# Optimization experiments

Hardware: AMD Instinct MI355X
Metric: run time of the kernel (lower is better)

## Reference

```python
import jax, jax.numpy as jnp
import numpy as np

V = 5023      # CoMA mesh vertices
K = 8         # avg neighbors per vertex
E = V * K     # edges
B = 64        # batch
C_IN = 3      # xyz
C_HID = 64    # conv width (layer_info)
M = 9         # kernel_size: number of weight matrices
LATENT = 128


def fsc_conv(x, src, dst, aw, u, c, W, b):
    """Feature-steered graph conv (translation invariant: v = -u).
    x: [B,V,C]; edge e: (i=src[e], j=dst[e]) with adjacency weight aw[e].
    y_i = b + sum_j a_ij * sum_m softmax_m(u_m.(x_i-x_j)+c_m) * (x_j @ W_m)
    """
    Bx, Vx, C = x.shape
    D = W.shape[2]
    xi = x[:, src]                                  # [B,E,C]
    xj = x[:, dst]                                  # [B,E,C]
    logits = jnp.einsum('bec,cm->bem', xi - xj, u) + c   # [B,E,M]
    att = jax.nn.softmax(logits, axis=-1) * aw[None, :, None]
    y = jnp.zeros((Bx, Vx, D), x.dtype)
    for m in range(W.shape[0]):                     # small fixed loop over M
        agg = jnp.zeros((Bx, Vx, C), x.dtype).at[:, src].add(att[:, :, m:m + 1] * xj)
        y = y + agg @ W[m]
    return y + b


def setup_inputs() -> dict:
    key = jax.random.key(0)
    ks = jax.random.split(key, 16)
    x = jax.random.normal(ks[0], (B, V, C_IN), jnp.float32)
    # mesh-like adjacency: each vertex i has K random neighbors, weight 1/K
    src = jnp.repeat(jnp.arange(V, dtype=jnp.int32), K)
    dst = jax.random.randint(ks[1], (E,), 0, V, dtype=jnp.int32)
    aw = jnp.full((E,), 1.0 / K, jnp.float32)
    g = lambda k, shp, fan: jax.random.normal(k, shp, jnp.float32) * np.float32(np.sqrt(2.0 / fan))
    # encoder conv params
    u_e = g(ks[2], (C_IN, M), C_IN + M)
    c_e = jnp.zeros((M,), jnp.float32)
    W_e = g(ks[3], (M, C_IN, C_HID), C_IN + C_HID)
    b_e = jnp.zeros((C_HID,), jnp.float32)
    # encoder latent dense: [V*C_HID, LATENT]
    W_enc = g(ks[4], (V * C_HID, LATENT), V * C_HID)
    b_enc = jnp.zeros((LATENT,), jnp.float32)
    # decoder latent dense: [LATENT, C_HID*V]
    W_dec = g(ks[5], (LATENT, C_HID * V), LATENT)
    b_dec = jnp.zeros((C_HID * V,), jnp.float32)
    # decoder conv params
    u_d = g(ks[6], (C_HID, M), C_HID + M)
    c_d = jnp.zeros((M,), jnp.float32)
    W_d = g(ks[7], (M, C_HID, C_IN), C_HID + C_IN)
    b_d = jnp.zeros((C_IN,), jnp.float32)
    return {'x': x, 'aw': aw, 'u_e': u_e, 'c_e': c_e, 'W_e': W_e, 'b_e': b_e,
            'W_enc': W_enc, 'b_enc': b_enc, 'W_dec': W_dec, 'b_dec': b_dec,
            'u_d': u_d, 'c_d': c_d, 'W_d': W_d, 'b_d': b_d,
            'src': src, 'dst': dst}


def reference(x, aw, u_e, c_e, W_e, b_e, W_enc, b_enc, W_dec, b_dec,
              u_d, c_d, W_d, b_d, src, dst):
    # Encoder: feature-steered conv -> relu -> flatten -> dense to latent
    h = jax.nn.relu(fsc_conv(x, src, dst, aw, u_e, c_e, W_e, b_e))   # [B,V,C_HID]
    z = h.reshape(h.shape[0], -1) @ W_enc + b_enc                    # [B,LATENT]
    # Decoder: dense -> reshape [B,V,C_HID] -> feature-steered conv -> relu
    d = (z @ W_dec + b_dec).reshape(z.shape[0], V, -1)               # [B,V,C_HID]
    out = jax.nn.relu(fsc_conv(d, src, dst, aw, u_d, c_d, W_d, b_d)) # [B,V,3]
    return out
```

## Files before the change

kernel.cpp:

```cpp
#include <hip/hip_runtime.h>

#define VN 5023
#define KN 8
#define BN 64
#define CIN 3
#define CH 64
#define MN 9
#define LAT 128
#define KTOT (VN*CH)
#define NBV (BN*VN)
#define KC 256
#define NCHUNK 1256
#define RED_G 8
#define RED_J 157
#define NXCD 8
#define DEC_TILES 1256
#define DEC_GRID 512

__global__ __launch_bounds__(256, 4) void k_conv1(
    const float* __restrict__ x, const float* __restrict__ aw,
    const int* __restrict__ dst,
    const float* __restrict__ u_e, const float* __restrict__ c_e,
    const float* __restrict__ W_e, const float* __restrict__ b_e,
    float* __restrict__ h)
{
  int t = blockIdx.x*256 + threadIdx.x;
  if (t >= NBV) return;
  int b = t / VN, v = t - b*VN;
  const float* xb = x + (size_t)b*VN*CIN;
  int e0 = v*KN;
  int4 j01 = *(const int4*)(dst + e0);
  int4 j23 = *(const int4*)(dst + e0 + 4);
  int jj[8] = {j01.x,j01.y,j01.z,j01.w, j23.x,j23.y,j23.z,j23.w};
  float4 a01 = *(const float4*)(aw + e0);
  float4 a23 = *(const float4*)(aw + e0 + 4);
  float awv[8] = {a01.x,a01.y,a01.z,a01.w, a23.x,a23.y,a23.z,a23.w};
  float xj0[8], xj1[8], xj2[8];
#pragma unroll
  for (int k=0;k<KN;k++){
    const float* xr = xb + (size_t)jj[k]*3;
    xj0[k]=xr[0]; xj1[k]=xr[1]; xj2[k]=xr[2];
  }
  __builtin_amdgcn_sched_barrier(0);
  float xi0 = xb[v*3+0], xi1 = xb[v*3+1], xi2 = xb[v*3+2];
  float Ti[MN];
#pragma unroll
  for (int m=0;m<MN;m++)
    Ti[m] = xi0*u_e[m] + xi1*u_e[MN+m] + xi2*u_e[2*MN+m] + c_e[m];
  float agg[27];
#pragma unroll
  for (int i=0;i<27;i++) agg[i]=0.f;
#pragma unroll
  for (int k=0;k<KN;k++){
    float lg[MN];
#pragma unroll
    for (int m=0;m<MN;m++)
      lg[m] = Ti[m] - (xj0[k]*u_e[m]+xj1[k]*u_e[MN+m]+xj2[k]*u_e[2*MN+m]);
    float mx = lg[0];
#pragma unroll
    for (int m=1;m<MN;m++) mx = fmaxf(mx, lg[m]);
    float ex[MN], s=0.f;
#pragma unroll
    for (int m=0;m<MN;m++){ ex[m] = __expf(lg[m]-mx); s += ex[m]; }
    float r = awv[k] / s;
#pragma unroll
    for (int m=0;m<MN;m++){
      float a = ex[m]*r;
      agg[m*3+0] += a*xj0[k]; agg[m*3+1] += a*xj1[k]; agg[m*3+2] += a*xj2[k];
    }
  }
  float* hr = h + (size_t)t*CH;
  for (int cc=0; cc<4; cc++){
    float y[16];
#pragma unroll
    for (int c=0;c<16;c++) y[c] = b_e[cc*16+c];
#pragma unroll
    for (int mc=0; mc<27; mc++){
      float a = agg[mc];
#pragma unroll
      for (int c=0;c<16;c++) y[c] += a * W_e[mc*CH + cc*16 + c];
    }
#pragma unroll
    for (int c=0;c<16;c+=4){
      float4 o = make_float4(fmaxf(y[c],0.f),fmaxf(y[c+1],0.f),
                             fmaxf(y[c+2],0.f),fmaxf(y[c+3],0.f));
      *(float4*)(hr + cc*16 + c) = o;
    }
  }
}

__global__ __launch_bounds__(256, 4) void k_enc(
    const float* __restrict__ h, const float* __restrict__ We,
    float* __restrict__ partial)
{
  __shared__ float wlds[2][32*128];
  __shared__ float hlds[2][32][68];
  int t = threadIdx.x;
  int blk = blockIdx.x;
  int lq = t & 15;
  int bq = t >> 4;
  float acc[8][4];
#pragma unroll
  for (int i=0;i<8;i++)
#pragma unroll
    for (int j=0;j<4;j++) acc[i][j]=0.f;
  int kbase0 = blk*KC;
  int ldb = t & 63;
  int seg = t >> 6;
  int nt0 = (blk == NCHUNK-1) ? 6 : 8;

  float4 wreg0, wreg1, wreg2, wreg3, hreg0, hreg1;
  {
    const float* wsrc = We + (size_t)kbase0*LAT;
    wreg0 = *(const float4*)(wsrc + 0*1024 + t*4);
    wreg1 = *(const float4*)(wsrc + 1*1024 + t*4);
    wreg2 = *(const float4*)(wsrc + 2*1024 + t*4);
    wreg3 = *(const float4*)(wsrc + 3*1024 + t*4);
    const float* hsrc = h + (size_t)ldb*KTOT + kbase0 + seg*8;
    hreg0 = *(const float4*)(hsrc);
    hreg1 = *(const float4*)(hsrc + 4);
    *(float4*)(&wlds[0][0*1024 + t*4]) = wreg0;
    *(float4*)(&wlds[0][1*1024 + t*4]) = wreg1;
    *(float4*)(&wlds[0][2*1024 + t*4]) = wreg2;
    *(float4*)(&wlds[0][3*1024 + t*4]) = wreg3;
    hlds[0][seg*8+0][ldb]=hreg0.x; hlds[0][seg*8+1][ldb]=hreg0.y;
    hlds[0][seg*8+2][ldb]=hreg0.z; hlds[0][seg*8+3][ldb]=hreg0.w;
    hlds[0][seg*8+4][ldb]=hreg1.x; hlds[0][seg*8+5][ldb]=hreg1.y;
    hlds[0][seg*8+6][ldb]=hreg1.z; hlds[0][seg*8+7][ldb]=hreg1.w;
  }
  __syncthreads();

  int cur = 0;
  for (int t0=0; t0<nt0; t0++){
    bool pf = (t0+1 < nt0);
    if (pf){
      int kbase = kbase0 + (t0+1)*32;
      const float* wsrc = We + (size_t)kbase*LAT;
      wreg0 = *(const float4*)(wsrc + 0*1024 + t*4);
      wreg1 = *(const float4*)(wsrc + 1*1024 + t*4);
      wreg2 = *(const float4*)(wsrc + 2*1024 + t*4);
      wreg3 = *(const float4*)(wsrc + 3*1024 + t*4);
      const float* hsrc = h + (size_t)ldb*KTOT + kbase + seg*8;
      hreg0 = *(const float4*)(hsrc);
      hreg1 = *(const float4*)(hsrc + 4);
    }
    __builtin_amdgcn_sched_barrier(0);
#pragma unroll 4
    for (int kk=0; kk<32; kk++){
      const float* wr = &wlds[cur][kk*128 + lq*8];
      float4 w0 = *(const float4*)wr;
      float4 w1 = *(const float4*)(wr+4);
      float4 z  = *(const float4*)(&hlds[cur][kk][bq*4]);
      float wv[8] = {w0.x,w0.y,w0.z,w0.w,w1.x,w1.y,w1.z,w1.w};
      float zv[4] = {z.x,z.y,z.z,z.w};
#pragma unroll
      for (int li=0;li<8;li++)
#pragma unroll
        for (int bi=0;bi<4;bi++) acc[li][bi] += wv[li]*zv[bi];
    }
    if (pf){
      int nb = cur^1;
      *(float4*)(&wlds[nb][0*1024 + t*4]) = wreg0;
      *(float4*)(&wlds[nb][1*1024 + t*4]) = wreg1;
      *(float4*)(&wlds[nb][2*1024 + t*4]) = wreg2;
      *(float4*)(&wlds[nb][3*1024 + t*4]) = wreg3;
      hlds[nb][seg*8+0][ldb]=hreg0.x; hlds[nb][seg*8+1][ldb]=hreg0.y;
      hlds[nb][seg*8+2][ldb]=hreg0.z; hlds[nb][seg*8+3][ldb]=hreg0.w;
      hlds[nb][seg*8+4][ldb]=hreg1.x; hlds[nb][seg*8+5][ldb]=hreg1.y;
      hlds[nb][seg*8+6][ldb]=hreg1.z; hlds[nb][seg*8+7][ldb]=hreg1.w;
    }
    __syncthreads();
    cur ^= 1;
  }
  float* pp = partial + (size_t)blk*(BN*LAT);
#pragma unroll
  for (int bi=0;bi<4;bi++){
    int b = bq*4+bi;
    float4 o0 = make_float4(acc[0][bi],acc[1][bi],acc[2][bi],acc[3][bi]);
    float4 o1 = make_float4(acc[4][bi],acc[5][bi],acc[6][bi],acc[7][bi]);
    *(float4*)(pp + b*LAT + lq*8)   = o0;
    *(float4*)(pp + b*LAT + lq*8+4) = o1;
  }
}

__global__ __launch_bounds__(256) void k_red1(
    const float* __restrict__ partial, float* __restrict__ partial2)
{
  int idx = blockIdx.x*256 + threadIdx.x;
  int g = blockIdx.y;
  float s = 0.f;
  for (int j=0;j<RED_J;j++)
    s += partial[(size_t)(g + RED_G*j)*(BN*LAT) + idx];
  partial2[(size_t)g*(BN*LAT) + idx] = s;
}

__global__ __launch_bounds__(256) void k_red2(
    const float* __restrict__ partial2, const float* __restrict__ b_enc,
    float* __restrict__ zT)
{
  int idx = blockIdx.x*256 + threadIdx.x;
  float s = 0.f;
#pragma unroll
  for (int g=0; g<RED_G; g++) s += partial2[(size_t)g*(BN*LAT) + idx];
  int b = idx >> 7, l = idx & 127;
  zT[l*BN + b] = s + b_enc[l];
}

__global__ __launch_bounds__(512, 2) void k_dec(
    const float* __restrict__ zT, const float* __restrict__ Wd,
    const float* __restrict__ b_dec, float* __restrict__ d)
{
  int t = threadIdx.x;
  int lane = t & 63;
  int wv = __builtin_amdgcn_readfirstlane(t >> 6);
  const float* zrow = zT + wv*8;
  for (int tile = blockIdx.x; tile < DEC_TILES; tile += DEC_GRID){
    int vc = tile*256 + lane*4;
    int vs = vc < (KTOT-4) ? vc : (KTOT-4);
    const float* wp = Wd + vs;
    float acc[4][8];
#pragma unroll
    for (int i=0;i<4;i++)
#pragma unroll
      for (int j=0;j<8;j++) acc[i][j]=0.f;

    float4 wA[8];
#pragma unroll
    for (int u=0;u<8;u++) wA[u] = *(const float4*)(wp + (size_t)u*KTOT);

    for (int l0=0; l0<LAT; l0+=8){
      float4 wB[8];
      bool pf = (l0+8 < LAT);
      if (pf){
#pragma unroll
        for (int u=0;u<8;u++)
          wB[u] = *(const float4*)(wp + (size_t)(l0+8+u)*KTOT);
      }
      __builtin_amdgcn_sched_barrier(0);
#pragma unroll
      for (int u=0;u<8;u++){
        int l = l0+u;
        float zv[8];
#pragma unroll
        for (int j=0;j<8;j++) zv[j] = zrow[l*BN + j];
        float wvv[4] = {wA[u].x,wA[u].y,wA[u].z,wA[u].w};
#pragma unroll
        for (int i=0;i<4;i++)
#pragma unroll
          for (int j=0;j<8;j++) acc[i][j] += wvv[i]*zv[j];
      }
      if (pf){
#pragma unroll
        for (int u=0;u<8;u++) wA[u] = wB[u];
      }
      __builtin_amdgcn_sched_barrier(0);
    }
    if (vc < KTOT){
      float4 bd = *(const float4*)(b_dec + vc);
#pragma unroll
      for (int j=0;j<8;j++){
        int b = wv*8 + j;
        float4 o = make_float4(acc[0][j]+bd.x, acc[1][j]+bd.y,
                               acc[2][j]+bd.z, acc[3][j]+bd.w);
        *(float4*)(d + (size_t)b*KTOT + vc) = o;
      }
    }
  }
}

__global__ __launch_bounds__(256, 4) void k_tg(
    const float* __restrict__ d, const float* __restrict__ u_d,
    const float* __restrict__ W_d, float* __restrict__ TG)
{
  int t = blockIdx.x*256 + threadIdx.x;
  if (t >= NBV) return;
  const float* drow = d + (size_t)t*CH;
  float T[MN], G[27];
#pragma unroll
  for (int m=0;m<MN;m++) T[m]=0.f;
#pragma unroll
  for (int i=0;i<27;i++) G[i]=0.f;
  for (int c0=0;c0<CH;c0+=4){
    float4 dv = *(const float4*)(drow+c0);
    float dvv[4] = {dv.x,dv.y,dv.z,dv.w};
#pragma unroll
    for (int j=0;j<4;j++){
      int c = c0+j;
      float xv = dvv[j];
#pragma unroll
      for (int m=0;m<MN;m++) T[m] += xv*u_d[c*MN+m];
#pragma unroll
      for (int m=0;m<MN;m++){
        G[m*3+0] += xv*W_d[(m*CH+c)*3+0];
        G[m*3+1] += xv*W_d[(m*CH+c)*3+1];
        G[m*3+2] += xv*W_d[(m*CH+c)*3+2];
      }
    }
  }
  float* tg = TG + (size_t)t*36;
  float rr[36] = {T[0],T[1],T[2],T[3],T[4],T[5],T[6],T[7],T[8],
                  G[0],G[1],G[2],G[3],G[4],G[5],G[6],G[7],G[8],
                  G[9],G[10],G[11],G[12],G[13],G[14],G[15],G[16],G[17],
                  G[18],G[19],G[20],G[21],G[22],G[23],G[24],G[25],G[26]};
#pragma unroll
  for (int i=0;i<36;i+=4)
    *(float4*)(tg+i) = make_float4(rr[i],rr[i+1],rr[i+2],rr[i+3]);
}

__global__ __launch_bounds__(256, 4) void k_att(
    const float* __restrict__ TG, const float* __restrict__ aw,
    const int* __restrict__ dst, const float* __restrict__ c_d,
    const float* __restrict__ b_d, float* __restrict__ out)
{
  int wg = blockIdx.x;
  int wgid = (wg & 7)*157 + (wg >> 3);
  int t = wgid*256 + threadIdx.x;
  if (t >= NBV) return;
  int b = t / VN, v = t - b*VN;
  const float* TGb = TG + (size_t)b*VN*36;
  int e0 = v*KN;
  int4 j01 = *(const int4*)(dst + e0);
  int4 j23 = *(const int4*)(dst + e0 + 4);
  int jj[8] = {j01.x,j01.y,j01.z,j01.w, j23.x,j23.y,j23.z,j23.w};
  float4 a01 = *(const float4*)(aw + e0);
  float4 a23 = *(const float4*)(aw + e0 + 4);
  float awv[8] = {a01.x,a01.y,a01.z,a01.w, a23.x,a23.y,a23.z,a23.w};
  float Ti[MN];
#pragma unroll
  for (int m=0;m<MN;m++) Ti[m] = TGb[(size_t)v*36+m] + c_d[m];
  float y0=0.f, y1=0.f, y2=0.f;
  float4 q[9];
  {
    const float* Rp = TGb + (size_t)jj[0]*36;
#pragma unroll
    for (int i=0;i<9;i++) q[i] = *(const float4*)(Rp + i*4);
  }
#pragma unroll
  for (int k=0;k<KN;k++){
    float4 p[9];
    if (k+1 < KN){
      const float* Rp = TGb + (size_t)jj[k+1]*36;
#pragma unroll
      for (int i=0;i<9;i++) p[i] = *(const float4*)(Rp + i*4);
    }
    float rr[36] = {q[0].x,q[0].y,q[0].z,q[0].w, q[1].x,q[1].y,q[1].z,q[1].w,
                    q[2].x,q[2].y,q[2].z,q[2].w, q[3].x,q[3].y,q[3].z,q[3].w,
                    q[4].x,q[4].y,q[4].z,q[4].w, q[5].x,q[5].y,q[5].z,q[5].w,
                    q[6].x,q[6].y,q[6].z,q[6].w, q[7].x,q[7].y,q[7].z,q[7].w,
                    q[8].x,q[8].y,q[8].z,q[8].w};
    float lg[MN];
#pragma unroll
    for (int m=0;m<MN;m++) lg[m] = Ti[m] - rr[m];
    float mx = lg[0];
#pragma unroll
    for (int m=1;m<MN;m++) mx = fmaxf(mx, lg[m]);
    float ex[MN], s=0.f;
#pragma unroll
    for (int m=0;m<MN;m++){ ex[m] = __expf(lg[m]-mx); s += ex[m]; }
    float sc = awv[k] / s;
#pragma unroll
    for (int m=0;m<MN;m++){
      float a = ex[m]*sc;
      y0 += a*rr[9+m*3+0]; y1 += a*rr[9+m*3+1]; y2 += a*rr[9+m*3+2];
    }
    if (k+1 < KN){
#pragma unroll
      for (int i=0;i<9;i++) q[i] = p[i];
    }
  }
  float* o = out + (size_t)t*3;
  o[0]=fmaxf(y0+b_d[0],0.f); o[1]=fmaxf(y1+b_d[1],0.f); o[2]=fmaxf(y2+b_d[2],0.f);
}

extern "C" void kernel_launch(void* const* d_in, const int* in_sizes, int n_in,
                              void* d_out, int out_size, void* d_ws, size_t ws_size,
                              hipStream_t stream) {
  const float* x     = (const float*)d_in[0];
  const float* aw    = (const float*)d_in[1];
  const float* u_e   = (const float*)d_in[2];
  const float* c_e   = (const float*)d_in[3];
  const float* W_e   = (const float*)d_in[4];
  const float* b_e   = (const float*)d_in[5];
  const float* W_enc = (const float*)d_in[6];
  const float* b_enc = (const float*)d_in[7];
  const float* W_dec = (const float*)d_in[8];
  const float* b_dec = (const float*)d_in[9];
  const float* u_d   = (const float*)d_in[10];
  const float* c_d   = (const float*)d_in[11];
  const float* W_d   = (const float*)d_in[12];
  const float* b_d   = (const float*)d_in[13];
  const int*   dst   = (const int*)d_in[15];
  float* out = (float*)d_out;

  char* ws = (char*)d_ws;
  float* hbuf = (float*)ws;
  size_t off1 = (size_t)NBV*CH*sizeof(float);
  float* partial = (float*)(ws + off1);
  float* TGbuf   = (float*)(ws + off1);
  size_t offz = off1 + (size_t)NCHUNK*(BN*LAT)*sizeof(float);
  float* zT       = (float*)(ws + offz);
  float* partial2 = (float*)(ws + offz + (size_t)(BN*LAT)*sizeof(float));

  int grid_bv = (NBV + 255)/256;

  k_conv1<<<grid_bv,256,0,stream>>>(x, aw, dst, u_e, c_e, W_e, b_e, hbuf);
  k_enc<<<NCHUNK,256,0,stream>>>(hbuf, W_enc, partial);
  dim3 gr1(32, RED_G);
  k_red1<<<gr1,256,0,stream>>>(partial, partial2);
  k_red2<<<32,256,0,stream>>>(partial2, b_enc, zT);
  k_dec<<<DEC_GRID,512,0,stream>>>(zT, W_dec, b_dec, hbuf);
  k_tg<<<grid_bv,256,0,stream>>>(hbuf, u_d, W_d, TGbuf);
  k_att<<<grid_bv,256,0,stream>>>(TGbuf, aw, dst, c_d, b_d, out);
}
```

Before: 360.8 us.

## Restructure decoder dense kernel with LDS double-buffered weight tiles and per-thread batch accumulators

```diff
diff --git a/kernel.cpp b/kernel.cpp
--- a/kernel.cpp
+++ b/kernel.cpp
@@ -14,8 +14,6 @@
 #define RED_G 8
 #define RED_J 157
 #define NXCD 8
-#define DEC_TILES 1256
-#define DEC_GRID 512
 
 __global__ __launch_bounds__(256, 4) void k_conv1(
     const float* __restrict__ x, const float* __restrict__ aw,
@@ -206,65 +204,78 @@
   zT[l*BN + b] = s + b_enc[l];
 }
 
-__global__ __launch_bounds__(512, 2) void k_dec(
+__global__ __launch_bounds__(256, 3) void k_dec(
     const float* __restrict__ zT, const float* __restrict__ Wd,
     const float* __restrict__ b_dec, float* __restrict__ d)
 {
+  __shared__ float wst[2][16*256];
   int t = threadIdx.x;
-  int lane = t & 63;
-  int wv = __builtin_amdgcn_readfirstlane(t >> 6);
-  const float* zrow = zT + wv*8;
-  for (int tile = blockIdx.x; tile < DEC_TILES; tile += DEC_GRID){
-    int vc = tile*256 + lane*4;
-    int vs = vc < (KTOT-4) ? vc : (KTOT-4);
-    const float* wp = Wd + vs;
-    float acc[4][8];
-#pragma unroll
-    for (int i=0;i<4;i++)
-#pragma unroll
-      for (int j=0;j<8;j++) acc[i][j]=0.f;
-
-    float4 wA[8];
-#pragma unroll
-    for (int u=0;u<8;u++) wA[u] = *(const float4*)(wp + (size_t)u*KTOT);
-
-    for (int l0=0; l0<LAT; l0+=8){
-      float4 wB[8];
-      bool pf = (l0+8 < LAT);
-      if (pf){
-#pragma unroll
-        for (int u=0;u<8;u++)
-          wB[u] = *(const float4*)(wp + (size_t)(l0+8+u)*KTOT);
+  int tile = blockIdx.x;
+  int vc = tile*256 + t;
+  float acc[BN];
+#pragma unroll
+  for (int j=0;j<BN;j++) acc[j]=0.f;
+
+  float4 sreg[4];
+  {
+#pragma unroll
+    for (int q=0;q<4;q++){
+      int f = q*256 + t;
+      int row = f>>6, col = (f&63)*4;
+      int g = tile*256 + col; g = g < (KTOT-4) ? g : (KTOT-4);
+      sreg[q] = *(const float4*)(Wd + (size_t)row*KTOT + g);
+    }
+#pragma unroll
+    for (int q=0;q<4;q++){
+      int f = q*256 + t;
+      int row = f>>6, col = (f&63)*4;
+      *(float4*)(&wst[0][row*256 + col]) = sreg[q];
+    }
+  }
+  __syncthreads();
+
+  int cur = 0;
+  for (int l0=0; l0<LAT; l0+=16){
+    bool pf = (l0+16 < LAT);
+    if (pf){
+#pragma unroll
+      for (int q=0;q<4;q++){
+        int f = q*256 + t;
+        int row = f>>6, col = (f&63)*4;
+        int g = tile*256 + col; g = g < (KTOT-4) ? g : (KTOT-4);
+        sreg[q] = *(const float4*)(Wd + (size_t)(l0+16+row)*KTOT + g);
       }
-      __builtin_amdgcn_sched_barrier(0);
-#pragma unroll
-      for (int u=0;u<8;u++){
-        int l = l0+u;
-        float zv[8];
-#pragma unroll
-        for (int j=0;j<8;j++) zv[j] = zrow[l*BN + j];
-        float wvv[4] = {wA[u].x,wA[u].y,wA[u].z,wA[u].w};
-#pragma unroll
-        for (int i=0;i<4;i++)
-#pragma unroll
-          for (int j=0;j<8;j++) acc[i][j] += wvv[i]*zv[j];
+    }
+    __builtin_amdgcn_sched_barrier(0);
+#pragma unroll
+    for (int lr=0; lr<16; lr++){
+      int l = l0 + lr;
+      float w = wst[cur][lr*256 + t];
+      const float* zr = zT + l*BN;
+#pragma unroll
+      for (int j4=0; j4<16; j4++){
+        float4 z = *(const float4*)(zr + j4*4);
+        acc[j4*4+0] += z.x*w; acc[j4*4+1] += z.y*w;
+        acc[j4*4+2] += z.z*w; acc[j4*4+3] += z.w*w;
       }
-      if (pf){
-#pragma unroll
-        for (int u=0;u<8;u++) wA[u] = wB[u];
+    }
+    if (pf){
+      int nb = cur^1;
+#pragma unroll
+      for (int q=0;q<4;q++){
+        int f = q*256 + t;
+        int row = f>>6, col = (f&63)*4;
+        *(float4*)(&wst[nb][row*256 + col]) = sreg[q];
       }
-      __builtin_amdgcn_sched_barrier(0);
-    }
-    if (vc < KTOT){
-      float4 bd = *(const float4*)(b_dec + vc);
-#pragma unroll
-      for (int j=0;j<8;j++){
-        int b = wv*8 + j;
-        float4 o = make_float4(acc[0][j]+bd.x, acc[1][j]+bd.y,
-                               acc[2][j]+bd.z, acc[3][j]+bd.w);
-        *(float4*)(d + (size_t)b*KTOT + vc) = o;
-      }
-    }
+    }
+    __syncthreads();
+    cur ^= 1;
+  }
+  if (vc < KTOT){
+    float bd = b_dec[vc];
+#pragma unroll
+    for (int j=0;j<BN;j++)
+      d[(size_t)j*KTOT + vc] = acc[j] + bd;
   }
 }
 
@@ -408,7 +419,8 @@
   dim3 gr1(32, RED_G);
   k_red1<<<gr1,256,0,stream>>>(partial, partial2);
   k_red2<<<32,256,0,stream>>>(partial2, b_enc, zT);
-  k_dec<<<DEC_GRID,512,0,stream>>>(zT, W_dec, b_dec, hbuf);
+  int grid_dec = (KTOT + 255)/256;
+  k_dec<<<grid_dec,256,0,stream>>>(zT, W_dec, b_dec, hbuf);
   k_tg<<<grid_bv,256,0,stream>>>(hbuf, u_d, W_d, TGbuf);
   k_att<<<grid_bv,256,0,stream>>>(TGbuf, aw, dst, c_d, b_d, out);
 }
```

After: 580.0 us. 60.8% more time.
